# Kernel optimization log

Hardware: AMD Instinct MI355X
Metric: run time of the kernel (lower is better)

## Reference

```python
import jax, jax.numpy as jnp
import numpy as np

N_EMBD = 1024
N_EXPERTS = 8
TOP_K = 2
B, T = 4, 2048


def setup_inputs() -> dict:
    key = jax.random.key(0)
    ks = jax.random.split(key, 8)
    C, E, H = N_EMBD, N_EXPERTS, 4 * N_EMBD
    s_in = 1.0 / np.sqrt(C)
    s_hid = 1.0 / np.sqrt(H)
    x = jax.random.normal(ks[0], (B, T, C), dtype=jnp.float32)
    # stacked expert FFN params: Linear(C,4C) -> ReLU -> Linear(4C,C)
    W1 = jax.random.uniform(ks[1], (E, C, H), minval=-s_in, maxval=s_in, dtype=jnp.float32)
    b1 = jax.random.uniform(ks[2], (E, H), minval=-s_in, maxval=s_in, dtype=jnp.float32)
    W2 = jax.random.uniform(ks[3], (E, H, C), minval=-s_hid, maxval=s_hid, dtype=jnp.float32)
    b2 = jax.random.uniform(ks[4], (E, C), minval=-s_hid, maxval=s_hid, dtype=jnp.float32)
    Wg = jax.random.uniform(ks[5], (C, E), minval=-s_in, maxval=s_in, dtype=jnp.float32)
    bg = jax.random.uniform(ks[6], (E,), minval=-s_in, maxval=s_in, dtype=jnp.float32)
    return {"x": x, "W1": W1, "b1": b1, "W2": W2, "b2": b2, "Wg": Wg, "bg": bg}


def reference(x, W1, b1, W2, b2, Wg, bg):
    # gate probabilities over experts: [B,T,E]
    gate_scores = jax.nn.softmax(jnp.einsum('btc,ce->bte', x, Wg) + bg, axis=-1)
    # dense all-expert FFN (dropout is identity in eval): [B,T,E,C]
    h = jax.nn.relu(jnp.einsum('btc,ech->bteh', x, W1) + b1)          # [B,T,E,4C]
    expert_out = jnp.einsum('bteh,ehc->btec', h, W2) + b2             # [B,T,E,C]
    # top-k gate selection + renormalized softmax over selected scores
    topk_scores, topk_idx = jax.lax.top_k(gate_scores, TOP_K)         # [B,T,k]
    top_probs = jax.nn.softmax(topk_scores, axis=-1)                  # [B,T,k]
    # gather selected experts' outputs: [B,T,k,C]
    sel = jnp.take_along_axis(expert_out, topk_idx[..., None], axis=2)
    out = jnp.sum(sel * top_probs[..., None], axis=2)                 # [B,T,C]
    return out
```

## Files before the change

### kernel.cpp

```cpp
#include <hip/hip_runtime.h>
#include <hip/hip_bf16.h>
#include <stdint.h>

#define E_    8
#define C_    1024
#define H_    4096
#define NTOK  8192
#define CAP   8192
#define MT_MAX 136

typedef __attribute__((ext_vector_type(8))) short bf16x8;
typedef __attribute__((ext_vector_type(4))) float f32x4;

__device__ __forceinline__ ushort f2bf(float f){
  union { float f; uint32_t u; } v; v.f = f;
  uint32_t r = v.u + 0x7fffu + ((v.u >> 16) & 1u);
  return (ushort)(r >> 16);
}

__device__ __forceinline__ void async16(const ushort* g, ushort* l){
  __builtin_amdgcn_global_load_lds(
      (const __attribute__((address_space(1))) void*)g,
      (__attribute__((address_space(3))) void*)l, 16, 0, 0);
}

__global__ void zero_counts(int* counts){
  if (threadIdx.x < E_) counts[threadIdx.x] = 0;
}

__global__ __launch_bounds__(256) void gate_kernel(
    const float* __restrict__ x, const float* __restrict__ Wg,
    const float* __restrict__ bg, const float* __restrict__ b2,
    float* __restrict__ out, int* __restrict__ counts,
    int* __restrict__ btok, float* __restrict__ bprob)
{
  int wave = threadIdx.x >> 6, lane = threadIdx.x & 63;
  int t = blockIdx.x * 4 + wave;
  const float* xr = x + (size_t)t * C_;

  float s[E_];
  #pragma unroll
  for (int e = 0; e < E_; ++e) s[e] = 0.f;
  for (int j = 0; j < 16; ++j){
    int c = j * 64 + lane;
    float xv = xr[c];
    const float* wr = Wg + c * E_;
    #pragma unroll
    for (int e = 0; e < E_; ++e) s[e] += xv * wr[e];
  }
  #pragma unroll
  for (int e = 0; e < E_; ++e){
    float v = s[e];
    for (int o = 32; o; o >>= 1) v += __shfl_xor(v, o);
    s[e] = v + bg[e];
  }
  float mx = s[0];
  #pragma unroll
  for (int e = 1; e < E_; ++e) mx = fmaxf(mx, s[e]);
  float g[E_]; float sum = 0.f;
  #pragma unroll
  for (int e = 0; e < E_; ++e){ g[e] = expf(s[e] - mx); sum += g[e]; }
  float inv = 1.f / sum;
  #pragma unroll
  for (int e = 0; e < E_; ++e) g[e] *= inv;
  int e0 = 0; float v0 = g[0];
  #pragma unroll
  for (int e = 1; e < E_; ++e) if (g[e] > v0){ v0 = g[e]; e0 = e; }
  int e1 = -1; float v1 = -1.f;
  #pragma unroll
  for (int e = 0; e < E_; ++e){ if (e == e0) continue; if (g[e] > v1){ v1 = g[e]; e1 = e; } }
  float q  = expf(v1 - v0);
  float p0 = 1.f / (1.f + q);
  float p1 = q / (1.f + q);

  const float* b2a = b2 + (size_t)e0 * C_;
  const float* b2b = b2 + (size_t)e1 * C_;
  float* orow = out + (size_t)t * C_;
  for (int j = 0; j < 16; ++j){
    int c = j * 64 + lane;
    orow[c] = p0 * b2a[c] + p1 * b2b[c];
  }
  if (lane == 0){
    int p = atomicAdd(&counts[e0], 1);
    btok[e0 * CAP + p] = t; bprob[e0 * CAP + p] = p0;
    p = atomicAdd(&counts[e1], 1);
    btok[e1 * CAP + p] = t; bprob[e1 * CAP + p] = p1;
  }
}

__global__ __launch_bounds__(256) void conv_x(const float* __restrict__ x, ushort* __restrict__ x16){
  size_t i = ((size_t)blockIdx.x * 256 + threadIdx.x) * 4;
  float4 v = *(const float4*)(x + i);
  ushort4 o;
  o.x = f2bf(v.x); o.y = f2bf(v.y); o.z = f2bf(v.z); o.w = f2bf(v.w);
  *(ushort4*)(x16 + i) = o;
}

__global__ __launch_bounds__(256) void transpose_w(const float* __restrict__ in, ushort* __restrict__ out,
                                                   int R, int S){
  __shared__ float t[64][65];
  int e  = blockIdx.z;
  int s0 = blockIdx.x * 64, r0 = blockIdx.y * 64;
  const float* ip = in  + (size_t)e * R * S;
  ushort*      op = out + (size_t)e * R * S;
  int cr = threadIdx.x >> 6;
  int cc = threadIdx.x & 63;
  #pragma unroll
  for (int i = 0; i < 16; ++i){
    int r = i * 4 + cr;
    t[r][cc] = ip[(size_t)(r0 + r) * S + s0 + cc];
  }
  __syncthreads();
  #pragma unroll
  for (int i = 0; i < 16; ++i){
    int s = i * 4 + cr;
    op[(size_t)(s0 + s) * R + r0 + cc] = f2bf(t[cc][s]);
  }
}

__global__ void setup_kernel(const int* __restrict__ counts, int* __restrict__ meta,
                             int* __restrict__ texp, int* __restrict__ tpos,
                             int* __restrict__ btok, float* __restrict__ bprob){
  __shared__ int toff[E_ + 1];
  if (threadIdx.x == 0){
    int to = 0;
    for (int e = 0; e < E_; ++e){ toff[e] = to; to += (counts[e] + 127) >> 7; }
    toff[E_] = to; meta[0] = to;
  }
  __syncthreads();
  int total = toff[E_];
  for (int i = threadIdx.x; i < MT_MAX; i += 256){
    if (i < total){
      int e = 0;
      while (e < E_ - 1 && i >= toff[e + 1]) ++e;
      texp[i] = e; tpos[i] = (i - toff[e]) * 128;
    } else { texp[i] = 0; tpos[i] = 0; }
  }
  for (int j = threadIdx.x; j < E_ * 128; j += 256){
    int e = j >> 7, r = j & 127;
    int c = counts[e];
    int padded = ((c + 127) >> 7) << 7;
    int pos = c + r;
    if (pos < padded){ btok[e * CAP + pos] = 0; bprob[e * CAP + pos] = 0.f; }
  }
}

__global__ __launch_bounds__(256) void gemm1(
    const ushort* __restrict__ x16, const ushort* __restrict__ w1t,
    const float* __restrict__ b1, ushort* __restrict__ h,
    const int* __restrict__ texp, const int* __restrict__ tpos,
    const int* __restrict__ btok, const int* __restrict__ meta)
{
  __shared__ ushort Al[128 * 32];
  __shared__ ushort Bl[128 * 32];
  __shared__ int toks[128];
  int mt = blockIdx.x;
  if (mt >= meta[0]) return;
  int tid = threadIdx.x, lane = tid & 63, wave = tid >> 6;
  int e = texp[mt], pb = tpos[mt];
  int n0 = blockIdx.y * 128;
  if (tid < 128) toks[tid] = btok[e * CAP + pb + tid];
  __syncthreads();

  int wr = wave >> 1, wc = wave & 1;
  int fr = lane & 15, kg = lane >> 4;
  const ushort* Bb = w1t + ((size_t)e * H_ + n0) * C_;

  f32x4 acc[4][4];
  #pragma unroll
  for (int m = 0; m < 4; ++m)
    #pragma unroll
    for (int n = 0; n < 4; ++n) acc[m][n] = 0.f;

  for (int k0 = 0; k0 < C_; k0 += 32){
    #pragma unroll
    for (int i = 0; i < 2; ++i){
      int ch = i * 256 + tid;
      int row = ch >> 2, k8 = ch & 3;
      async16(x16 + (size_t)toks[row] * C_ + k0 + k8 * 8, Al + ch * 8);
    }
    #pragma unroll
    for (int i = 0; i < 2; ++i){
      int ch = i * 256 + tid;
      int col = ch >> 2, k8 = ch & 3;
      async16(Bb + (size_t)col * C_ + k0 + k8 * 8, Bl + ch * 8);
    }
    __syncthreads();
    bf16x8 af[4], bfr[4];
    #pragma unroll
    for (int m = 0; m < 4; ++m) af[m]  = *(const bf16x8*)(Al + (wr * 64 + m * 16 + fr) * 32 + kg * 8);
    #pragma unroll
    for (int n = 0; n < 4; ++n) bfr[n] = *(const bf16x8*)(Bl + (wc * 64 + n * 16 + fr) * 32 + kg * 8);
    #pragma unroll
    for (int m = 0; m < 4; ++m)
      #pragma unroll
      for (int n = 0; n < 4; ++n)
        acc[m][n] = __builtin_amdgcn_mfma_f32_16x16x32_bf16(af[m], bfr[n], acc[m][n], 0, 0, 0);
    __syncthreads();
  }

  int fq = lane >> 4;
  size_t hb = (size_t)mt * 128;
  #pragma unroll
  for (int n = 0; n < 4; ++n){
    int nc = n0 + wc * 64 + n * 16 + fr;
    float bv = b1[(size_t)e * H_ + nc];
    #pragma unroll
    for (int m = 0; m < 4; ++m){
      int rbase = wr * 64 + m * 16 + fq * 4;
      #pragma unroll
      for (int r = 0; r < 4; ++r){
        float v = acc[m][n][r] + bv;
        h[(hb + rbase + r) * H_ + nc] = f2bf(v > 0.f ? v : 0.f);
      }
    }
  }
}

__global__ __launch_bounds__(256) void gemm2(
    const ushort* __restrict__ h, const ushort* __restrict__ w2t,
    float* __restrict__ out,
    const int* __restrict__ texp, const int* __restrict__ tpos,
    const int* __restrict__ btok, const float* __restrict__ bprob,
    const int* __restrict__ meta)
{
  __shared__ ushort Al[128 * 32];
  __shared__ ushort Bl[128 * 32];
  __shared__ int toks[128];
  __shared__ float probs[128];
  int mt = blockIdx.x;
  if (mt >= meta[0]) return;
  int tid = threadIdx.x, lane = tid & 63, wave = tid >> 6;
  int e = texp[mt], pb = tpos[mt];
  int n0 = blockIdx.y * 128;
  if (tid < 128){
    toks[tid]  = btok[e * CAP + pb + tid];
    probs[tid] = bprob[e * CAP + pb + tid];
  }
  __syncthreads();

  int wr = wave >> 1, wc = wave & 1;
  int fr = lane & 15, kg = lane >> 4;
  const ushort* Bb = w2t + ((size_t)e * C_ + n0) * H_;
  const ushort* Ab = h + (size_t)mt * 128 * H_;

  f32x4 acc[4][4];
  #pragma unroll
  for (int m = 0; m < 4; ++m)
    #pragma unroll
    for (int n = 0; n < 4; ++n) acc[m][n] = 0.f;

  for (int k0 = 0; k0 < H_; k0 += 32){
    #pragma unroll
    for (int i = 0; i < 2; ++i){
      int ch = i * 256 + tid;
      int row = ch >> 2, k8 = ch & 3;
      async16(Ab + (size_t)row * H_ + k0 + k8 * 8, Al + ch * 8);
    }
    #pragma unroll
    for (int i = 0; i < 2; ++i){
      int ch = i * 256 + tid;
      int col = ch >> 2, k8 = ch & 3;
      async16(Bb + (size_t)col * H_ + k0 + k8 * 8, Bl + ch * 8);
    }
    __syncthreads();
    bf16x8 af[4], bfr[4];
    #pragma unroll
    for (int m = 0; m < 4; ++m) af[m]  = *(const bf16x8*)(Al + (wr * 64 + m * 16 + fr) * 32 + kg * 8);
    #pragma unroll
    for (int n = 0; n < 4; ++n) bfr[n] = *(const bf16x8*)(Bl + (wc * 64 + n * 16 + fr) * 32 + kg * 8);
    #pragma unroll
    for (int m = 0; m < 4; ++m)
      #pragma unroll
      for (int n = 0; n < 4; ++n)
        acc[m][n] = __builtin_amdgcn_mfma_f32_16x16x32_bf16(af[m], bfr[n], acc[m][n], 0, 0, 0);
    __syncthreads();
  }

  int fq = lane >> 4;
  #pragma unroll
  for (int n = 0; n < 4; ++n){
    int nc = n0 + wc * 64 + n * 16 + fr;
    #pragma unroll
    for (int m = 0; m < 4; ++m){
      int rbase = wr * 64 + m * 16 + fq * 4;
      #pragma unroll
      for (int r = 0; r < 4; ++r){
        int row = rbase + r;
        atomicAdd(out + (size_t)toks[row] * C_ + nc, probs[row] * acc[m][n][r]);
      }
    }
  }
}

extern "C" void kernel_launch(void* const* d_in, const int* in_sizes, int n_in,
                              void* d_out, int out_size, void* d_ws, size_t ws_size,
                              hipStream_t stream)
{
  const float* x  = (const float*)d_in[0];
  const float* W1 = (const float*)d_in[1];
  const float* b1 = (const float*)d_in[2];
  const float* W2 = (const float*)d_in[3];
  const float* b2 = (const float*)d_in[4];
  const float* Wg = (const float*)d_in[5];
  const float* bg = (const float*)d_in[6];
  float* out = (float*)d_out;

  char* ws = (char*)d_ws;
  size_t off = 0;
  auto alloc = [&](size_t b){ size_t r = off; off += (b + 4095) & ~(size_t)4095; return r; };
  int*    counts = (int*)   (ws + alloc(E_ * 4));
  int*    meta   = (int*)   (ws + alloc(64));
  int*    texp   = (int*)   (ws + alloc(MT_MAX * 4));
  int*    tpos   = (int*)   (ws + alloc(MT_MAX * 4));
  int*    btok   = (int*)   (ws + alloc((size_t)E_ * CAP * 4));
  float*  bprob  = (float*) (ws + alloc((size_t)E_ * CAP * 4));
  ushort* x16    = (ushort*)(ws + alloc((size_t)NTOK * C_ * 2));
  ushort* w1t    = (ushort*)(ws + alloc((size_t)E_ * C_ * H_ * 2));
  ushort* w2t    = (ushort*)(ws + alloc((size_t)E_ * C_ * H_ * 2));
  ushort* h      = (ushort*)(ws + alloc((size_t)MT_MAX * 128 * H_ * 2));
  (void)ws_size; (void)in_sizes; (void)n_in; (void)out_size;

  zero_counts<<<dim3(1), dim3(64), 0, stream>>>(counts);
  gate_kernel<<<dim3(NTOK / 4), dim3(256), 0, stream>>>(x, Wg, bg, b2, out, counts, btok, bprob);
  conv_x<<<dim3((NTOK * C_) / (4 * 256)), dim3(256), 0, stream>>>(x, x16);
  transpose_w<<<dim3(H_ / 64, C_ / 64, E_), dim3(256), 0, stream>>>(W1, w1t, C_, H_);
  transpose_w<<<dim3(C_ / 64, H_ / 64, E_), dim3(256), 0, stream>>>(W2, w2t, H_, C_);
  setup_kernel<<<dim3(1), dim3(256), 0, stream>>>(counts, meta, texp, tpos, btok, bprob);
  gemm1<<<dim3(MT_MAX, H_ / 128), dim3(256), 0, stream>>>(x16, w1t, b1, h, texp, tpos, btok, meta);
  gemm2<<<dim3(MT_MAX, C_ / 128), dim3(256), 0, stream>>>(h, w2t, out, texp, tpos, btok, bprob, meta);
}
```

Measured before the change: 1.168 ms.

## Double-buffer LDS tiles in expert GEMMs and fuse bf16 conversion into gate

Both expert GEMM kernels now use two LDS buffers. The next K-tile's async global-to-LDS loads are issued before the MFMAs on the current tile, and one barrier per iteration is removed. Row base pointers are precomputed once outside the K loop. The separate x-to-bf16 conversion kernel is folded into the gate kernel, which already reads x, saving a launch and a full pass over x. The cost is doubled LDS per block, which may reduce occupancy.

```diff
diff --git a/kernel.cpp b/kernel.cpp
--- a/kernel.cpp
+++ b/kernel.cpp
@@ -32,11 +32,13 @@
     const float* __restrict__ x, const float* __restrict__ Wg,
     const float* __restrict__ bg, const float* __restrict__ b2,
     float* __restrict__ out, int* __restrict__ counts,
-    int* __restrict__ btok, float* __restrict__ bprob)
+    int* __restrict__ btok, float* __restrict__ bprob,
+    ushort* __restrict__ x16)
 {
   int wave = threadIdx.x >> 6, lane = threadIdx.x & 63;
   int t = blockIdx.x * 4 + wave;
   const float* xr = x + (size_t)t * C_;
+  ushort* x16r = x16 + (size_t)t * C_;
 
   float s[E_];
   #pragma unroll
@@ -44,6 +46,7 @@
   for (int j = 0; j < 16; ++j){
     int c = j * 64 + lane;
     float xv = xr[c];
+    x16r[c] = f2bf(xv);
     const float* wr = Wg + c * E_;
     #pragma unroll
     for (int e = 0; e < E_; ++e) s[e] += xv * wr[e];
@@ -86,14 +89,6 @@
     p = atomicAdd(&counts[e1], 1);
     btok[e1 * CAP + p] = t; bprob[e1 * CAP + p] = p1;
   }
-}
-
-__global__ __launch_bounds__(256) void conv_x(const float* __restrict__ x, ushort* __restrict__ x16){
-  size_t i = ((size_t)blockIdx.x * 256 + threadIdx.x) * 4;
-  float4 v = *(const float4*)(x + i);
-  ushort4 o;
-  o.x = f2bf(v.x); o.y = f2bf(v.y); o.z = f2bf(v.z); o.w = f2bf(v.w);
-  *(ushort4*)(x16 + i) = o;
 }
 
 __global__ __launch_bounds__(256) void transpose_w(const float* __restrict__ in, ushort* __restrict__ out,
@@ -151,8 +146,8 @@
     const int* __restrict__ texp, const int* __restrict__ tpos,
     const int* __restrict__ btok, const int* __restrict__ meta)
 {
-  __shared__ ushort Al[128 * 32];
-  __shared__ ushort Bl[128 * 32];
+  __shared__ ushort Al[2][128 * 32];
+  __shared__ ushort Bl[2][128 * 32];
   __shared__ int toks[128];
   int mt = blockIdx.x;
   if (mt >= meta[0]) return;
@@ -166,37 +161,62 @@
   int fr = lane & 15, kg = lane >> 4;
   const ushort* Bb = w1t + ((size_t)e * H_ + n0) * C_;
 
+  const ushort* pA[2]; const ushort* pB[2];
+  #pragma unroll
+  for (int i = 0; i < 2; ++i){
+    int ch = i * 256 + tid;
+    pA[i] = x16 + (size_t)toks[ch >> 2] * C_ + (ch & 3) * 8;
+    pB[i] = Bb  + (size_t)(ch >> 2)     * C_ + (ch & 3) * 8;
+  }
+
   f32x4 acc[4][4];
   #pragma unroll
   for (int m = 0; m < 4; ++m)
     #pragma unroll
     for (int n = 0; n < 4; ++n) acc[m][n] = 0.f;
 
-  for (int k0 = 0; k0 < C_; k0 += 32){
+  #pragma unroll
+  for (int i = 0; i < 2; ++i){
+    int ch = i * 256 + tid;
+    async16(pA[i], &Al[0][ch * 8]);
+    async16(pB[i], &Bl[0][ch * 8]);
+  }
+  __syncthreads();
+
+  const int NT = C_ / 32;
+  int cur = 0;
+  for (int t = 0; t < NT - 1; ++t){
+    int k0n = (t + 1) * 32;
     #pragma unroll
     for (int i = 0; i < 2; ++i){
       int ch = i * 256 + tid;
-      int row = ch >> 2, k8 = ch & 3;
-      async16(x16 + (size_t)toks[row] * C_ + k0 + k8 * 8, Al + ch * 8);
+      async16(pA[i] + k0n, &Al[cur ^ 1][ch * 8]);
+      async16(pB[i] + k0n, &Bl[cur ^ 1][ch * 8]);
     }
-    #pragma unroll
-    for (int i = 0; i < 2; ++i){
-      int ch = i * 256 + tid;
-      int col = ch >> 2, k8 = ch & 3;
-      async16(Bb + (size_t)col * C_ + k0 + k8 * 8, Bl + ch * 8);
-    }
-    __syncthreads();
     bf16x8 af[4], bfr[4];
     #pragma unroll
-    for (int m = 0; m < 4; ++m) af[m]  = *(const bf16x8*)(Al + (wr * 64 + m * 16 + fr) * 32 + kg * 8);
-    #pragma unroll
-    for (int n = 0; n < 4; ++n) bfr[n] = *(const bf16x8*)(Bl + (wc * 64 + n * 16 + fr) * 32 + kg * 8);
+    for (int m = 0; m < 4; ++m) af[m]  = *(const bf16x8*)(&Al[cur][(wr * 64 + m * 16 + fr) * 32 + kg * 8]);
+    #pragma unroll
+    for (int n = 0; n < 4; ++n) bfr[n] = *(const bf16x8*)(&Bl[cur][(wc * 64 + n * 16 + fr) * 32 + kg * 8]);
     #pragma unroll
     for (int m = 0; m < 4; ++m)
       #pragma unroll
       for (int n = 0; n < 4; ++n)
         acc[m][n] = __builtin_amdgcn_mfma_f32_16x16x32_bf16(af[m], bfr[n], acc[m][n], 0, 0, 0);
     __syncthreads();
+    cur ^= 1;
+  }
+  {
+    bf16x8 af[4], bfr[4];
+    #pragma unroll
+    for (int m = 0; m < 4; ++m) af[m]  = *(const bf16x8*)(&Al[cur][(wr * 64 + m * 16 + fr) * 32 + kg * 8]);
+    #pragma unroll
+    for (int n = 0; n < 4; ++n) bfr[n] = *(const bf16x8*)(&Bl[cur][(wc * 64 + n * 16 + fr) * 32 + kg * 8]);
+    #pragma unroll
+    for (int m = 0; m < 4; ++m)
+      #pragma unroll
+      for (int n = 0; n < 4; ++n)
+        acc[m][n] = __builtin_amdgcn_mfma_f32_16x16x32_bf16(af[m], bfr[n], acc[m][n], 0, 0, 0);
   }
 
   int fq = lane >> 4;
@@ -224,8 +244,8 @@
     const int* __restrict__ btok, const float* __restrict__ bprob,
     const int* __restrict__ meta)
 {
-  __shared__ ushort Al[128 * 32];
-  __shared__ ushort Bl[128 * 32];
+  __shared__ ushort Al[2][128 * 32];
+  __shared__ ushort Bl[2][128 * 32];
   __shared__ int toks[128];
   __shared__ float probs[128];
   int mt = blockIdx.x;
@@ -244,37 +264,62 @@
   const ushort* Bb = w2t + ((size_t)e * C_ + n0) * H_;
   const ushort* Ab = h + (size_t)mt * 128 * H_;
 
+  const ushort* pA[2]; const ushort* pB[2];
+  #pragma unroll
+  for (int i = 0; i < 2; ++i){
+    int ch = i * 256 + tid;
+    pA[i] = Ab + (size_t)(ch >> 2) * H_ + (ch & 3) * 8;
+    pB[i] = Bb + (size_t)(ch >> 2) * H_ + (ch & 3) * 8;
+  }
+
   f32x4 acc[4][4];
   #pragma unroll
   for (int m = 0; m < 4; ++m)
     #pragma unroll
     for (int n = 0; n < 4; ++n) acc[m][n] = 0.f;
 
-  for (int k0 = 0; k0 < H_; k0 += 32){
+  #pragma unroll
+  for (int i = 0; i < 2; ++i){
+    int ch = i * 256 + tid;
+    async16(pA[i], &Al[0][ch * 8]);
+    async16(pB[i], &Bl[0][ch * 8]);
+  }
+  __syncthreads();
+
+  const int NT = H_ / 32;
+  int cur = 0;
+  for (int t = 0; t < NT - 1; ++t){
+    int k0n = (t + 1) * 32;
     #pragma unroll
     for (int i = 0; i < 2; ++i){
       int ch = i * 256 + tid;
-      int row = ch >> 2, k8 = ch & 3;
-      async16(Ab + (size_t)row * H_ + k0 + k8 * 8, Al + ch * 8);
+      async16(pA[i] + k0n, &Al[cur ^ 1][ch * 8]);
+      async16(pB[i] + k0n, &Bl[cur ^ 1][ch * 8]);
     }
-    #pragma unroll
-    for (int i = 0; i < 2; ++i){
-      int ch = i * 256 + tid;
-      int col = ch >> 2, k8 = ch & 3;
-      async16(Bb + (size_t)col * H_ + k0 + k8 * 8, Bl + ch * 8);
-    }
-    __syncthreads();
     bf16x8 af[4], bfr[4];
     #pragma unroll
-    for (int m = 0; m < 4; ++m) af[m]  = *(const bf16x8*)(Al + (wr * 64 + m * 16 + fr) * 32 + kg * 8);
-    #pragma unroll
-    for (int n = 0; n < 4; ++n) bfr[n] = *(const bf16x8*)(Bl + (wc * 64 + n * 16 + fr) * 32 + kg * 8);
+    for (int m = 0; m < 4; ++m) af[m]  = *(const bf16x8*)(&Al[cur][(wr * 64 + m * 16 + fr) * 32 + kg * 8]);
+    #pragma unroll
+    for (int n = 0; n < 4; ++n) bfr[n] = *(const bf16x8*)(&Bl[cur][(wc * 64 + n * 16 + fr) * 32 + kg * 8]);
     #pragma unroll
     for (int m = 0; m < 4; ++m)
       #pragma unroll
       for (int n = 0; n < 4; ++n)
         acc[m][n] = __builtin_amdgcn_mfma_f32_16x16x32_bf16(af[m], bfr[n], acc[m][n], 0, 0, 0);
     __syncthreads();
+    cur ^= 1;
+  }
+  {
+    bf16x8 af[4], bfr[4];
+    #pragma unroll
+    for (int m = 0; m < 4; ++m) af[m]  = *(const bf16x8*)(&Al[cur][(wr * 64 + m * 16 + fr) * 32 + kg * 8]);
+    #pragma unroll
+    for (int n = 0; n < 4; ++n) bfr[n] = *(const bf16x8*)(&Bl[cur][(wc * 64 + n * 16 + fr) * 32 + kg * 8]);
+    #pragma unroll
+    for (int m = 0; m < 4; ++m)
+      #pragma unroll
+      for (int n = 0; n < 4; ++n)
+        acc[m][n] = __builtin_amdgcn_mfma_f32_16x16x32_bf16(af[m], bfr[n], acc[m][n], 0, 0, 0);
   }
 
   int fq = lane >> 4;
@@ -322,8 +367,7 @@
   (void)ws_size; (void)in_sizes; (void)n_in; (void)out_size;
 
   zero_counts<<<dim3(1), dim3(64), 0, stream>>>(counts);
-  gate_kernel<<<dim3(NTOK / 4), dim3(256), 0, stream>>>(x, Wg, bg, b2, out, counts, btok, bprob);
-  conv_x<<<dim3((NTOK * C_) / (4 * 256)), dim3(256), 0, stream>>>(x, x16);
+  gate_kernel<<<dim3(NTOK / 4), dim3(256), 0, stream>>>(x, Wg, bg, b2, out, counts, btok, bprob, x16);
   transpose_w<<<dim3(H_ / 64, C_ / 64, E_), dim3(256), 0, stream>>>(W1, w1t, C_, H_);
   transpose_w<<<dim3(C_ / 64, H_ / 64, E_), dim3(256), 0, stream>>>(W2, w2t, H_, C_);
   setup_kernel<<<dim3(1), dim3(256), 0, stream>>>(counts, meta, texp, tpos, btok, bprob);
```

Result: faster. 1.112 ms (-4.8%).
